# Kernel optimization log

Hardware: AMD Instinct MI355X
Metric: run time of the kernel (lower is better)

Reference implementation:

```python
import jax, jax.numpy as jnp
import numpy as np

N_STATE = 2048   # n_state_neurons
N_U = 64         # n_features_U
N_Y = 128        # n_features_Y
PAST = 64        # past_horizon
FORE = 16        # forecast_horizon
BATCH = 256


def setup_inputs() -> dict:
    key = jax.random.key(0)
    k1, k2, k3, k4 = jax.random.split(key, 4)
    U = jax.random.normal(k1, (PAST + FORE, BATCH, N_U), dtype=jnp.float32)
    Y = jax.random.normal(k2, (PAST, BATCH, N_Y), dtype=jnp.float32)
    # Transition matrix of the bias-free Linear A: cat(state, U) -> state.
    # Stored as (in, out) so the step is x @ A (same math as torch Linear with W = A.T).
    A = jax.random.normal(k3, (N_STATE + N_U, N_STATE), dtype=jnp.float32) * 0.02
    init_state = jax.random.normal(k4, (1, N_STATE), dtype=jnp.float32)
    return {"U": U, "Y": Y, "A": A, "init_state": init_state}


def reference(U, Y, A, init_state):
    past = Y.shape[0]
    batch = Y.shape[1]
    n_y = Y.shape[2]
    state0 = jnp.broadcast_to(init_state, (batch, init_state.shape[1]))

    # Past horizon: expectation = first n_y state components; error = expectation - Y.
    # Teacher forcing (p=1): subtract error from those components (i.e. force them to Y),
    # append known features U, then state' = A(tanh(cat(post_state, U))).
    def past_step(state, inp):
        u, y = inp
        err = state[:, :n_y] - y                    # (B, n_y) past error
        post = state.at[:, :n_y].set(y)             # full teacher forcing
        x = jnp.tanh(jnp.concatenate([post, u], axis=1))
        return x @ A, err

    state, past_err = jax.lax.scan(past_step, state0, (U[:past], Y))

    # Forecast horizon: no observation, output the expectation itself.
    def fore_step(state, u):
        expectation = state[:, :n_y]
        x = jnp.tanh(jnp.concatenate([state, u], axis=1))
        return x @ A, expectation

    _, forecast = jax.lax.scan(fore_step, state, U[past:])

    # (past + forecast, batch, n_y): past errors then forecasts, as in torch.cat.
    return jnp.concatenate([past_err, forecast], axis=0)
```

## Files before the change

kernel.cpp:

```cpp
#include <hip/hip_runtime.h>

typedef float f32x4 __attribute__((ext_vector_type(4)));
typedef int   i32x4 __attribute__((ext_vector_type(4)));

#define KDIM   2112
#define NST    2048
#define NYD    128
#define NUD    64
#define BATCHD 256

__device__ __forceinline__ unsigned short f2bf(float f) {
  unsigned int u = __builtin_bit_cast(unsigned int, f);
  u = (u + 0x7FFFu + ((u >> 16) & 1u)) >> 16;
  return (unsigned short)u;
}

__device__ __forceinline__ float tanh_fast(float x) {
  float ax = __builtin_fabsf(x);
  float e  = __expf(-2.0f * ax);
  float r  = (1.0f - e) / (1.0f + e);
  return __builtin_copysignf(r, x);
}

__device__ __forceinline__ void gl_lds16(const unsigned short* g, unsigned short* l) {
  __builtin_amdgcn_global_load_lds(
      (const __attribute__((address_space(1))) unsigned int*)g,
      (__attribute__((address_space(3))) unsigned int*)l, 16, 0, 0);
}

__global__ void k_prepA(const float* __restrict__ A, unsigned short* __restrict__ At) {
  __shared__ float tile[64][65];
  int nbase = blockIdx.x * 64;
  int kbase = blockIdx.y * 64;
  int tx = threadIdx.x & 63;
  int ty = threadIdx.x >> 6;
  for (int r = 0; r < 64; r += 4)
    tile[r + ty][tx] = A[(size_t)(kbase + r + ty) * NST + nbase + tx];
  __syncthreads();
  for (int r = 0; r < 64; r += 4) {
    int ni = r + ty;
    At[(size_t)(nbase + ni) * KDIM + kbase + tx] = f2bf(tile[tx][ni]);
  }
}

__global__ void k_prepX0(const float* __restrict__ U, const float* __restrict__ Y,
                         const float* __restrict__ init, unsigned short* __restrict__ X0,
                         float* __restrict__ out) {
  int m = blockIdx.x;
  int c = blockIdx.y * 256 + threadIdx.x;
  if (c >= KDIM) return;
  float v;
  if (c < NYD) {
    float y = Y[(size_t)m * NYD + c];
    out[(size_t)m * NYD + c] = init[c] - y;
    v = y;
  } else if (c < NST) {
    v = init[c];
  } else {
    v = U[(size_t)m * NUD + (c - NST)];
  }
  X0[(size_t)m * KDIM + c] = f2bf(tanh_fast(v));
}

#define MFMA(ACC, A_, B_) \
  asm("v_mfma_f32_16x16x32_bf16 %0, %1, %2, %0" : "+v"(ACC) : "v"(A_), "v"(B_))

__global__ void __launch_bounds__(64) k_step(const unsigned short* __restrict__ Xc,
                                             unsigned short* __restrict__ Xn,
                                             const unsigned short* __restrict__ At,
                                             const float* __restrict__ U,
                                             const float* __restrict__ Y,
                                             float* __restrict__ out, int s) {
  __shared__ __align__(16) unsigned short lds[6144];
  int bid = blockIdx.x;
  int xcd = bid & 7, idx = bid >> 3;
  int j = xcd * 4 + (idx & 3);
  int i = idx >> 2;
  int Mb = i * 32, Nb = j * 64;
  int lane = threadIdx.x;

  int sr = lane >> 2;
  int g8 = (((lane & 3) ^ ((lane >> 3) & 3)) << 3);
  const unsigned short* xs0 = Xc + (size_t)(Mb +      sr) * KDIM + g8;
  const unsigned short* xs1 = Xc + (size_t)(Mb + 16 + sr) * KDIM + g8;
  const unsigned short* bs0 = At + (size_t)(Nb +      sr) * KDIM + g8;
  const unsigned short* bs1 = At + (size_t)(Nb + 16 + sr) * KDIM + g8;
  const unsigned short* bs2 = At + (size_t)(Nb + 32 + sr) * KDIM + g8;
  const unsigned short* bs3 = At + (size_t)(Nb + 48 + sr) * KDIM + g8;

#define STAGE(it2, b) do { int kb = (it2) << 5;                       \
    gl_lds16(xs0 + kb, lds + (b) * 1024);                             \
    gl_lds16(xs1 + kb, lds + (b) * 1024 + 512);                       \
    gl_lds16(bs0 + kb, lds + 2048 + (b) * 2048);                      \
    gl_lds16(bs1 + kb, lds + 2048 + (b) * 2048 + 512);                \
    gl_lds16(bs2 + kb, lds + 2048 + (b) * 2048 + 1024);               \
    gl_lds16(bs3 + kb, lds + 2048 + (b) * 2048 + 1536);               \
  } while (0)

  int row = lane & 15, kh = lane >> 4;
  int fo = row * 32 + (((kh ^ ((row >> 1) & 3))) << 3);

  f32x4 acc00 = {0.f,0.f,0.f,0.f}, acc01 = {0.f,0.f,0.f,0.f};
  f32x4 acc02 = {0.f,0.f,0.f,0.f}, acc03 = {0.f,0.f,0.f,0.f};
  f32x4 acc10 = {0.f,0.f,0.f,0.f}, acc11 = {0.f,0.f,0.f,0.f};
  f32x4 acc12 = {0.f,0.f,0.f,0.f}, acc13 = {0.f,0.f,0.f,0.f};

  STAGE(0, 0);
  STAGE(1, 1);

#define ITER(it, VM) do {                                             \
    asm volatile("s_waitcnt vmcnt(" #VM ")" ::: "memory");            \
    __builtin_amdgcn_sched_barrier(0);                                \
    const unsigned short* xb = lds + ((it) & 1) * 1024;               \
    const unsigned short* bb = lds + 2048 + ((it) & 1) * 2048;        \
    i32x4 a0 = *(const i32x4*)(xb + fo);                              \
    i32x4 a1 = *(const i32x4*)(xb + 512 + fo);                        \
    i32x4 b0 = *(const i32x4*)(bb + fo);                              \
    i32x4 b1 = *(const i32x4*)(bb + 512 + fo);                        \
    i32x4 b2 = *(const i32x4*)(bb + 1024 + fo);                       \
    i32x4 b3 = *(const i32x4*)(bb + 1536 + fo);                       \
    MFMA(acc00, a0, b0); MFMA(acc01, a0, b1);                         \
    MFMA(acc02, a0, b2); MFMA(acc03, a0, b3);                         \
    MFMA(acc10, a1, b0); MFMA(acc11, a1, b1);                         \
    MFMA(acc12, a1, b2); MFMA(acc13, a1, b3);                         \
    asm volatile("s_waitcnt lgkmcnt(0)" ::: "memory");                \
    __builtin_amdgcn_sched_barrier(0);                                \
    if ((it) + 2 < 66) STAGE((it) + 2, (it) & 1);                     \
  } while (0)

#pragma unroll 2
  for (int it = 0; it < 65; ++it) ITER(it, 6);
  ITER(65, 0);

  int col16 = lane & 15, row4 = (lane >> 4) << 2;
  bool past = s < 64;

#define EPI(ACC, MB, CB) do {                                         \
    _Pragma("unroll")                                                 \
    for (int r = 0; r < 4; ++r) {                                     \
      int m = Mb + (MB) * 16 + row4 + r;                              \
      int n = Nb + (CB) * 16 + col16;                                 \
      float v = ACC[r]; float xv;                                     \
      if (n < NYD) {                                                  \
        size_t oo = ((size_t)s * BATCHD + m) * NYD + n;               \
        if (past) { float y = Y[oo]; out[oo] = v - y; xv = tanh_fast(y); } \
        else      { out[oo] = v; xv = tanh_fast(v); }                 \
      } else xv = tanh_fast(v);                                       \
      Xn[(size_t)m * KDIM + n] = f2bf(xv);                            \
    }                                                                 \
  } while (0)

  EPI(acc00, 0, 0); EPI(acc01, 0, 1); EPI(acc02, 0, 2); EPI(acc03, 0, 3);
  EPI(acc10, 1, 0); EPI(acc11, 1, 1); EPI(acc12, 1, 2); EPI(acc13, 1, 3);

  if (j == 0) {
#pragma unroll 4
    for (int rr = 0; rr < 32; ++rr) {
      int m = Mb + rr;
      float u = U[((size_t)s * BATCHD + m) * NUD + lane];
      Xn[(size_t)m * KDIM + NST + lane] = f2bf(tanh_fast(u));
    }
  }
}

extern "C" void kernel_launch(void* const* d_in, const int* in_sizes, int n_in,
                              void* d_out, int out_size, void* d_ws, size_t ws_size,
                              hipStream_t stream) {
  (void)in_sizes; (void)n_in; (void)out_size; (void)ws_size;
  const float* U    = (const float*)d_in[0];
  const float* Y    = (const float*)d_in[1];
  const float* A    = (const float*)d_in[2];
  const float* init = (const float*)d_in[3];
  float* out = (float*)d_out;

  char* ws = (char*)d_ws;
  unsigned short* At = (unsigned short*)ws;
  unsigned short* X0 = (unsigned short*)(ws + 8650752);
  unsigned short* X1 = (unsigned short*)(ws + 8650752 + 1081344);

  k_prepA<<<dim3(32, 33), 256, 0, stream>>>(A, At);
  k_prepX0<<<dim3(256, 9), 256, 0, stream>>>(U, Y, init, X0, out);

  for (int t = 0; t < 79; ++t) {
    const unsigned short* xc = (t & 1) ? X1 : X0;
    unsigned short*       xn = (t & 1) ? X0 : X1;
    k_step<<<256, 64, 0, stream>>>(xc, xn, At, U, Y, out, t + 1);
  }
}
```

Baseline: 2.052 ms.

## Replace per-step launches with persistent kernel holding A in registers and flag sync

The 79 separate step launches are replaced by one persistent kernel of 256 workgroups. Each workgroup keeps its slice of the bf16 transition matrix resident in registers across all steps and splits K in two halves, with partial sums exchanged through global memory. Steps are ordered with fine-grained atomic flags and a triple-buffered state instead of kernel boundaries, and tanh(U) is precomputed for all steps up front. This removes launch overhead and the repeated re-reading of A each step. In exchange it relies on all 256 workgroups being co-resident, and the spin-waits carry a bounded timeout that could break silently.

```diff
diff --git a/kernel.cpp b/kernel.cpp
--- a/kernel.cpp
+++ b/kernel.cpp
@@ -1,18 +1,20 @@
 #include <hip/hip_runtime.h>
 
 typedef float f32x4 __attribute__((ext_vector_type(4)));
-typedef int   i32x4 __attribute__((ext_vector_type(4)));
-
+typedef short s16x8 __attribute__((ext_vector_type(8)));
+typedef unsigned short u16;
+
+#define NST    2048
 #define KDIM   2112
-#define NST    2048
 #define NYD    128
 #define NUD    64
-#define BATCHD 256
-
-__device__ __forceinline__ unsigned short f2bf(float f) {
+#define BD     256
+#define NSTEP  80
+
+__device__ __forceinline__ u16 f2bf(float f) {
   unsigned int u = __builtin_bit_cast(unsigned int, f);
   u = (u + 0x7FFFu + ((u >> 16) & 1u)) >> 16;
-  return (unsigned short)u;
+  return (u16)u;
 }
 
 __device__ __forceinline__ float tanh_fast(float x) {
@@ -22,13 +24,30 @@
   return __builtin_copysignf(r, x);
 }
 
-__device__ __forceinline__ void gl_lds16(const unsigned short* g, unsigned short* l) {
+__device__ __forceinline__ void gl_lds16(const u16* g, u16* l) {
   __builtin_amdgcn_global_load_lds(
       (const __attribute__((address_space(1))) unsigned int*)g,
       (__attribute__((address_space(3))) unsigned int*)l, 16, 0, 0);
 }
 
-__global__ void k_prepA(const float* __restrict__ A, unsigned short* __restrict__ At) {
+__device__ __forceinline__ f32x4 MF(s16x8 a, s16x8 b, f32x4 c) {
+  return __builtin_amdgcn_mfma_f32_16x16x32_bf16(a, b, c, 0, 0, 0);
+}
+
+__device__ __forceinline__ void waitge(int* p, int v) {
+  int g = 0;
+  while (__hip_atomic_load(p, __ATOMIC_RELAXED, __HIP_MEMORY_SCOPE_AGENT) < v) {
+    __builtin_amdgcn_s_sleep(2);
+    if (++g > (1 << 24)) break;
+  }
+}
+
+__global__ void k_init(int* flags) {
+  int i = blockIdx.x * 256 + threadIdx.x;
+  if (i < 7424) flags[i] = (i < 128 && (i & 15) == 0) ? 16 : 0;
+}
+
+__global__ void k_prepA(const float* __restrict__ A, u16* __restrict__ At) {
   __shared__ float tile[64][65];
   int nbase = blockIdx.x * 64;
   int kbase = blockIdx.y * 64;
@@ -43,124 +62,183 @@
   }
 }
 
-__global__ void k_prepX0(const float* __restrict__ U, const float* __restrict__ Y,
-                         const float* __restrict__ init, unsigned short* __restrict__ X0,
-                         float* __restrict__ out) {
+__global__ void k_prepX0(const float* __restrict__ Y, const float* __restrict__ init,
+                         u16* __restrict__ X1, float* __restrict__ out) {
   int m = blockIdx.x;
   int c = blockIdx.y * 256 + threadIdx.x;
-  if (c >= KDIM) return;
   float v;
   if (c < NYD) {
     float y = Y[(size_t)m * NYD + c];
     out[(size_t)m * NYD + c] = init[c] - y;
     v = y;
-  } else if (c < NST) {
-    v = init[c];
-  } else {
-    v = U[(size_t)m * NUD + (c - NST)];
-  }
-  X0[(size_t)m * KDIM + c] = f2bf(tanh_fast(v));
-}
-
-#define MFMA(ACC, A_, B_) \
-  asm("v_mfma_f32_16x16x32_bf16 %0, %1, %2, %0" : "+v"(ACC) : "v"(A_), "v"(B_))
-
-__global__ void __launch_bounds__(64) k_step(const unsigned short* __restrict__ Xc,
-                                             unsigned short* __restrict__ Xn,
-                                             const unsigned short* __restrict__ At,
-                                             const float* __restrict__ U,
-                                             const float* __restrict__ Y,
-                                             float* __restrict__ out, int s) {
-  __shared__ __align__(16) unsigned short lds[6144];
-  int bid = blockIdx.x;
-  int xcd = bid & 7, idx = bid >> 3;
-  int j = xcd * 4 + (idx & 3);
-  int i = idx >> 2;
-  int Mb = i * 32, Nb = j * 64;
-  int lane = threadIdx.x;
-
-  int sr = lane >> 2;
-  int g8 = (((lane & 3) ^ ((lane >> 3) & 3)) << 3);
-  const unsigned short* xs0 = Xc + (size_t)(Mb +      sr) * KDIM + g8;
-  const unsigned short* xs1 = Xc + (size_t)(Mb + 16 + sr) * KDIM + g8;
-  const unsigned short* bs0 = At + (size_t)(Nb +      sr) * KDIM + g8;
-  const unsigned short* bs1 = At + (size_t)(Nb + 16 + sr) * KDIM + g8;
-  const unsigned short* bs2 = At + (size_t)(Nb + 32 + sr) * KDIM + g8;
-  const unsigned short* bs3 = At + (size_t)(Nb + 48 + sr) * KDIM + g8;
-
-#define STAGE(it2, b) do { int kb = (it2) << 5;                       \
-    gl_lds16(xs0 + kb, lds + (b) * 1024);                             \
-    gl_lds16(xs1 + kb, lds + (b) * 1024 + 512);                       \
-    gl_lds16(bs0 + kb, lds + 2048 + (b) * 2048);                      \
-    gl_lds16(bs1 + kb, lds + 2048 + (b) * 2048 + 512);                \
-    gl_lds16(bs2 + kb, lds + 2048 + (b) * 2048 + 1024);               \
-    gl_lds16(bs3 + kb, lds + 2048 + (b) * 2048 + 1536);               \
+  } else v = init[c];
+  X1[(size_t)m * NST + c] = f2bf(tanh_fast(v));
+}
+
+__global__ void k_prepXu(const float* __restrict__ U, u16* __restrict__ Xu) {
+  int i = blockIdx.x * 256 + threadIdx.x;
+  if (i < NSTEP * BD * NUD) Xu[i] = f2bf(tanh_fast(U[i]));
+}
+
+__global__ void __launch_bounds__(256, 1)
+k_persist(const u16* __restrict__ At, u16* __restrict__ Xp0, u16* __restrict__ Xp1,
+          u16* __restrict__ Xp2, const u16* __restrict__ Xu,
+          float* __restrict__ partial, int* rdycnt, int* pseq, int* consumed,
+          int* xdone, const float* __restrict__ Y, float* __restrict__ out) {
+  __shared__ u16 ldsX[3][4096];
+
+  const int w = blockIdx.x;
+  const int j = w & 31, ks = (w >> 5) & 1, mb = w >> 6;
+  const int tid = threadIdx.x, wv = tid >> 6, lane = tid & 63;
+  const int l15 = lane & 15, lg = lane >> 4;
+  const int wr = wv >> 1, wc = wv & 1;
+  const int m0 = mb * 64, n0 = j * 64, k0 = ks * 1024;
+  const int fidx = j * 4 + mb;
+  const int rdy = (mb * 2 + ks) * 16;
+  const int rel = (mb * 2 + (j >> 4)) * 16;
+
+  s16x8 b[68];
+  {
+    const u16* base = At + (size_t)(n0 + wc * 32 + l15) * KDIM + lg * 8;
+#pragma unroll
+    for (int kc = 0; kc < 32; ++kc) {
+      b[kc * 2 + 0] = *(const s16x8*)(base + k0 + kc * 32);
+      b[kc * 2 + 1] = *(const s16x8*)(base + (size_t)16 * KDIM + k0 + kc * 32);
+    }
+    if (ks) {
+#pragma unroll
+      for (int c = 0; c < 2; ++c) {
+        b[64 + c * 2 + 0] = *(const s16x8*)(base + 2048 + c * 32);
+        b[64 + c * 2 + 1] = *(const s16x8*)(base + (size_t)16 * KDIM + 2048 + c * 32);
+      }
+    }
+  }
+
+#define STAGE_PAIR(P, B_) do {                                                      \
+    const u16* s_ = xsrc + (size_t)(m0 + (tid >> 2)) * NST + k0 + (P) * 64 +        \
+                    (tid & 3) * 8;                                                  \
+    gl_lds16(s_,      &ldsX[B_][(tid >> 6) * 512]);                                 \
+    gl_lds16(s_ + 32, &ldsX[B_][2048 + (tid >> 6) * 512]);                          \
   } while (0)
 
-  int row = lane & 15, kh = lane >> 4;
-  int fo = row * 32 + (((kh ^ ((row >> 1) & 3))) << 3);
-
-  f32x4 acc00 = {0.f,0.f,0.f,0.f}, acc01 = {0.f,0.f,0.f,0.f};
-  f32x4 acc02 = {0.f,0.f,0.f,0.f}, acc03 = {0.f,0.f,0.f,0.f};
-  f32x4 acc10 = {0.f,0.f,0.f,0.f}, acc11 = {0.f,0.f,0.f,0.f};
-  f32x4 acc12 = {0.f,0.f,0.f,0.f}, acc13 = {0.f,0.f,0.f,0.f};
-
-  STAGE(0, 0);
-  STAGE(1, 1);
-
-#define ITER(it, VM) do {                                             \
-    asm volatile("s_waitcnt vmcnt(" #VM ")" ::: "memory");            \
-    __builtin_amdgcn_sched_barrier(0);                                \
-    const unsigned short* xb = lds + ((it) & 1) * 1024;               \
-    const unsigned short* bb = lds + 2048 + ((it) & 1) * 2048;        \
-    i32x4 a0 = *(const i32x4*)(xb + fo);                              \
-    i32x4 a1 = *(const i32x4*)(xb + 512 + fo);                        \
-    i32x4 b0 = *(const i32x4*)(bb + fo);                              \
-    i32x4 b1 = *(const i32x4*)(bb + 512 + fo);                        \
-    i32x4 b2 = *(const i32x4*)(bb + 1024 + fo);                       \
-    i32x4 b3 = *(const i32x4*)(bb + 1536 + fo);                       \
-    MFMA(acc00, a0, b0); MFMA(acc01, a0, b1);                         \
-    MFMA(acc02, a0, b2); MFMA(acc03, a0, b3);                         \
-    MFMA(acc10, a1, b0); MFMA(acc11, a1, b1);                         \
-    MFMA(acc12, a1, b2); MFMA(acc13, a1, b3);                         \
-    asm volatile("s_waitcnt lgkmcnt(0)" ::: "memory");                \
-    __builtin_amdgcn_sched_barrier(0);                                \
-    if ((it) + 2 < 66) STAGE((it) + 2, (it) & 1);                     \
+#define PAIR_BODY(P, VM) do {                                                       \
+    asm volatile("s_waitcnt vmcnt(" #VM ")" ::: "memory");                          \
+    __builtin_amdgcn_sched_barrier(0);                                              \
+    __builtin_amdgcn_s_barrier();                                                   \
+    __builtin_amdgcn_sched_barrier(0);                                              \
+    const u16* xq = &ldsX[(P) % 3][0];                                              \
+    s16x8 a00 = *(const s16x8*)(xq + (wr * 32 + l15) * 32 + lg * 8);                \
+    s16x8 a10 = *(const s16x8*)(xq + (wr * 32 + 16 + l15) * 32 + lg * 8);           \
+    s16x8 a01 = *(const s16x8*)(xq + 2048 + (wr * 32 + l15) * 32 + lg * 8);         \
+    s16x8 a11 = *(const s16x8*)(xq + 2048 + (wr * 32 + 16 + l15) * 32 + lg * 8);    \
+    acc00 = MF(a00, b[(P) * 4 + 0], acc00);                                         \
+    acc01 = MF(a00, b[(P) * 4 + 1], acc01);                                         \
+    acc10 = MF(a10, b[(P) * 4 + 0], acc10);                                         \
+    acc11 = MF(a10, b[(P) * 4 + 1], acc11);                                         \
+    acc00 = MF(a01, b[(P) * 4 + 2], acc00);                                         \
+    acc01 = MF(a01, b[(P) * 4 + 3], acc01);                                         \
+    acc10 = MF(a11, b[(P) * 4 + 2], acc10);                                         \
+    acc11 = MF(a11, b[(P) * 4 + 3], acc11);                                         \
+    __builtin_amdgcn_sched_barrier(0);                                              \
+    if ((P) <= 13) STAGE_PAIR((P) + 2, ((P) + 2) % 3);                              \
+    __builtin_amdgcn_sched_barrier(0);                                              \
   } while (0)
 
-#pragma unroll 2
-  for (int it = 0; it < 65; ++it) ITER(it, 6);
-  ITER(65, 0);
-
-  int col16 = lane & 15, row4 = (lane >> 4) << 2;
-  bool past = s < 64;
-
-#define EPI(ACC, MB, CB) do {                                         \
-    _Pragma("unroll")                                                 \
-    for (int r = 0; r < 4; ++r) {                                     \
-      int m = Mb + (MB) * 16 + row4 + r;                              \
-      int n = Nb + (CB) * 16 + col16;                                 \
-      float v = ACC[r]; float xv;                                     \
-      if (n < NYD) {                                                  \
-        size_t oo = ((size_t)s * BATCHD + m) * NYD + n;               \
-        if (past) { float y = Y[oo]; out[oo] = v - y; xv = tanh_fast(y); } \
-        else      { out[oo] = v; xv = tanh_fast(v); }                 \
-      } else xv = tanh_fast(v);                                       \
-      Xn[(size_t)m * KDIM + n] = f2bf(xv);                            \
-    }                                                                 \
-  } while (0)
-
-  EPI(acc00, 0, 0); EPI(acc01, 0, 1); EPI(acc02, 0, 2); EPI(acc03, 0, 3);
-  EPI(acc10, 1, 0); EPI(acc11, 1, 1); EPI(acc12, 1, 2); EPI(acc13, 1, 3);
-
-  if (j == 0) {
-#pragma unroll 4
-    for (int rr = 0; rr < 32; ++rr) {
-      int m = Mb + rr;
-      float u = U[((size_t)s * BATCHD + m) * NUD + lane];
-      Xn[(size_t)m * KDIM + NST + lane] = f2bf(tanh_fast(u));
-    }
-  }
+  for (int tau = 1; tau < NSTEP; ++tau) {
+    int r3 = tau % 3, n3 = (tau + 1) % 3;
+    const u16* xsrc = r3 == 0 ? Xp0 : r3 == 1 ? Xp1 : Xp2;
+    u16* xdst = n3 == 0 ? Xp0 : n3 == 1 ? Xp1 : Xp2;
+
+    waitge(&rdycnt[rdy], 16 * tau);
+    __builtin_amdgcn_fence(__ATOMIC_ACQUIRE, "agent");
+
+    STAGE_PAIR(0, 0);
+    STAGE_PAIR(1, 1);
+
+    f32x4 acc00 = {0.f, 0.f, 0.f, 0.f}, acc01 = {0.f, 0.f, 0.f, 0.f};
+    f32x4 acc10 = {0.f, 0.f, 0.f, 0.f}, acc11 = {0.f, 0.f, 0.f, 0.f};
+
+    PAIR_BODY(0, 2);  PAIR_BODY(1, 2);  PAIR_BODY(2, 2);  PAIR_BODY(3, 2);
+    PAIR_BODY(4, 2);  PAIR_BODY(5, 2);  PAIR_BODY(6, 2);  PAIR_BODY(7, 2);
+    PAIR_BODY(8, 2);  PAIR_BODY(9, 2);  PAIR_BODY(10, 2); PAIR_BODY(11, 2);
+    PAIR_BODY(12, 2); PAIR_BODY(13, 2); PAIR_BODY(14, 2); PAIR_BODY(15, 0);
+
+    if (ks) {
+      const u16* ub = Xu + (size_t)(tau - 1) * (BD * NUD) +
+                      (size_t)(m0 + wr * 32 + l15) * NUD + lg * 8;
+      s16x8 u00 = *(const s16x8*)(ub);
+      s16x8 u10 = *(const s16x8*)(ub + 16 * NUD);
+      s16x8 u01 = *(const s16x8*)(ub + 32);
+      s16x8 u11 = *(const s16x8*)(ub + 16 * NUD + 32);
+      acc00 = MF(u00, b[64], acc00); acc01 = MF(u00, b[65], acc01);
+      acc10 = MF(u10, b[64], acc10); acc11 = MF(u10, b[65], acc11);
+      acc00 = MF(u01, b[66], acc00); acc01 = MF(u01, b[67], acc01);
+      acc10 = MF(u11, b[66], acc10); acc11 = MF(u11, b[67], acc11);
+    }
+
+    __syncthreads();
+    if (tid == 0)
+      __hip_atomic_fetch_add(&xdone[tau * 16], 1, __ATOMIC_RELAXED,
+                             __HIP_MEMORY_SCOPE_AGENT);
+
+    if (ks) {
+      waitge(&consumed[fidx * 16], tau - 2);
+      __builtin_amdgcn_fence(__ATOMIC_ACQUIRE, "agent");
+      float* pb = partial + ((size_t)fidx * 2 + (tau & 1)) * 4096 + tid * 16;
+      *(f32x4*)(pb + 0)  = acc00;
+      *(f32x4*)(pb + 4)  = acc01;
+      *(f32x4*)(pb + 8)  = acc10;
+      *(f32x4*)(pb + 12) = acc11;
+      __syncthreads();
+      if (tid == 0) {
+        __builtin_amdgcn_fence(__ATOMIC_RELEASE, "agent");
+        __hip_atomic_store(&pseq[fidx * 16], tau, __ATOMIC_RELAXED,
+                           __HIP_MEMORY_SCOPE_AGENT);
+      }
+    } else {
+      waitge(&pseq[fidx * 16], tau);
+      __builtin_amdgcn_fence(__ATOMIC_ACQUIRE, "agent");
+      const float* pb = partial + ((size_t)fidx * 2 + (tau & 1)) * 4096 + tid * 16;
+      f32x4 p0 = *(const f32x4*)(pb + 0);
+      f32x4 p1 = *(const f32x4*)(pb + 4);
+      f32x4 p2 = *(const f32x4*)(pb + 8);
+      f32x4 p3 = *(const f32x4*)(pb + 12);
+      acc00 += p0; acc01 += p1; acc10 += p2; acc11 += p3;
+      __syncthreads();
+      if (tid == 0) {
+        __builtin_amdgcn_fence(__ATOMIC_RELEASE, "agent");
+        __hip_atomic_store(&consumed[fidx * 16], tau, __ATOMIC_RELAXED,
+                           __HIP_MEMORY_SCOPE_AGENT);
+      }
+      if (tau >= 3) waitge(&xdone[(tau - 2) * 16], 256);
+
+      bool past = tau < 64;
+#define EPI1(ACC, F, G) do {                                                        \
+      _Pragma("unroll")                                                             \
+      for (int r = 0; r < 4; ++r) {                                                 \
+        int m = m0 + wr * 32 + (F) * 16 + lg * 4 + r;                               \
+        int col = n0 + wc * 32 + (G) * 16 + l15;                                    \
+        float v = ACC[r]; float xv;                                                 \
+        if (col < NYD) {                                                            \
+          size_t oo = ((size_t)tau * BD + m) * NYD + col;                           \
+          if (past) { float y = Y[oo]; out[oo] = v - y; xv = tanh_fast(y); }        \
+          else      { out[oo] = v; xv = tanh_fast(v); }                             \
+        } else xv = tanh_fast(v);                                                   \
+        xdst[(size_t)m * NST + col] = f2bf(xv);                                     \
+      }                                                                             \
+    } while (0)
+      EPI1(acc00, 0, 0); EPI1(acc01, 0, 1); EPI1(acc10, 1, 0); EPI1(acc11, 1, 1);
+      __syncthreads();
+      if (tid == 0) {
+        __builtin_amdgcn_fence(__ATOMIC_RELEASE, "agent");
+        __hip_atomic_fetch_add(&rdycnt[rel], 1, __ATOMIC_RELAXED,
+                               __HIP_MEMORY_SCOPE_AGENT);
+      }
+    }
+  }
+#undef STAGE_PAIR
+#undef PAIR_BODY
+#undef EPI1
 }
 
 extern "C" void kernel_launch(void* const* d_in, const int* in_sizes, int n_in,
@@ -174,16 +252,23 @@
   float* out = (float*)d_out;
 
   char* ws = (char*)d_ws;
-  unsigned short* At = (unsigned short*)ws;
-  unsigned short* X0 = (unsigned short*)(ws + 8650752);
-  unsigned short* X1 = (unsigned short*)(ws + 8650752 + 1081344);
-
+  int* flags    = (int*)ws;
+  int* rdycnt   = flags;
+  int* pseq     = flags + 2048;
+  int* consumed = flags + 4096;
+  int* xdone    = flags + 6144;
+  u16* At = (u16*)(ws + 32768);
+  u16* X0 = (u16*)(ws + 8683520);
+  u16* X1 = (u16*)(ws + 8683520 + 1048576);
+  u16* X2 = (u16*)(ws + 8683520 + 2097152);
+  u16* Xu = (u16*)(ws + 11829248);
+  float* partial = (float*)(ws + 14450688);
+
+  k_init<<<29, 256, 0, stream>>>(flags);
   k_prepA<<<dim3(32, 33), 256, 0, stream>>>(A, At);
-  k_prepX0<<<dim3(256, 9), 256, 0, stream>>>(U, Y, init, X0, out);
-
-  for (int t = 0; t < 79; ++t) {
-    const unsigned short* xc = (t & 1) ? X1 : X0;
-    unsigned short*       xn = (t & 1) ? X0 : X1;
-    k_step<<<256, 64, 0, stream>>>(xc, xn, At, U, Y, out, t + 1);
-  }
-}
+  k_prepX0<<<dim3(256, 8), 256, 0, stream>>>(Y, init, X1, out);
+  k_prepXu<<<(NSTEP * BD * NUD + 255) / 256, 256, 0, stream>>>(U, Xu);
+
+  k_persist<<<256, 256, 73728, stream>>>(At, X0, X1, X2, Xu, partial,
+                                         rdycnt, pseq, consumed, xdone, Y, out);
+}
```

After: 2.722 ms. 1.33x slower.
